# Optimization experiments

Measured on AMD Instinct MI355X. Metric: run time of the kernel, lower is better.

Reference implementation:

```python
import jax, jax.numpy as jnp
import numpy as np

B, A, NBH, F, G, H = 8, 512, 64, 128, 50, 8
DH = F // H
CUTOFF = 5.0


def setup_inputs() -> dict:
    key = jax.random.key(0)
    ks = jax.random.split(key, 13)
    x = jax.random.normal(ks[0], (B, A, F), jnp.float32)
    e = jax.random.normal(ks[1], (B, A, F), jnp.float32)
    t = jax.random.normal(ks[2], (B, F), jnp.float32)
    # distances in [0, 1.2*cutoff] so some pairs fall outside the cutoff
    r_ij = jax.random.uniform(ks[3], (B, A, NBH), jnp.float32) * (1.2 * CUTOFF)
    f_ij = jax.random.normal(ks[4], (B, A, NBH, G), jnp.float32)
    neighbors = jax.random.randint(ks[5], (B, A, NBH), 0, A, jnp.int32)
    neighbor_mask = jax.random.randint(ks[6], (B, A, NBH), 0, 2, jnp.int32).astype(bool)
    sF = 1.0 / np.sqrt(F).astype(np.float32)
    W_filt = jax.random.normal(ks[7], (G, F), jnp.float32) * (1.0 / np.sqrt(G).astype(np.float32))
    b_filt = jnp.zeros((F,), jnp.float32)
    Wq = jax.random.normal(ks[8], (F, F), jnp.float32) * sF
    Wk = jax.random.normal(ks[9], (F, F), jnp.float32) * sF
    Wv = jax.random.normal(ks[10], (F, F), jnp.float32) * sF
    Wo = jax.random.normal(ks[11], (F, F), jnp.float32) * sF
    bo = jnp.zeros((F,), jnp.float32)
    return dict(e=e, x=x, t=t, r_ij=r_ij, f_ij=f_ij,
                W_filt=W_filt, b_filt=b_filt, Wq=Wq, Wk=Wk, Wv=Wv, Wo=Wo, bo=bo,
                neighbors=neighbors, neighbor_mask=neighbor_mask)


def reference(e, x, t, r_ij, f_ij, W_filt, b_filt, Wq, Wk, Wv, Wo, bo,
              neighbors, neighbor_mask):
    # ---- filter network + cosine cutoff: W (B, A, NBH, F) ----
    W = f_ij @ W_filt + b_filt
    C = 0.5 * (jnp.cos(jnp.pi * r_ij / CUTOFF) + 1.0)
    C = C * (r_ij < CUTOFF).astype(x.dtype)           # (B, A, NBH)
    W = W * C[..., None]

    # ---- neighbor gather: nbh (B, A, NBH, F) ----
    bidx = jnp.arange(B)[:, None, None]
    nbh = x[bidx, neighbors]                           # irregular gather
    nbh = nbh * W                                      # filter-modulated messages

    # ---- EgoAttention: central atom queries its neighbors ----
    q = (x @ Wq).reshape(B, A, H, DH)                  # bahd
    k = (nbh @ Wk).reshape(B, A, NBH, H, DH)           # banhd
    v = (nbh @ Wv).reshape(B, A, NBH, H, DH)
    scale = np.float32(1.0 / np.sqrt(DH))
    scores = jnp.einsum('bahd,banhd->bahn', q, k) * scale
    scores = jnp.where(neighbor_mask[:, :, None, :], scores, jnp.float32(-1e9))
    attn = jax.nn.softmax(scores, axis=-1)             # over neighbors
    msg = jnp.einsum('bahn,banhd->bahd', attn, v).reshape(B, A, F)
    v_out = msg @ Wo + bo

    # ---- residual (apply_transition_function=False branch) ----
    return x + v_out
```

## Files before the change

kernel.cpp:

```cpp
#include <hip/hip_runtime.h>
#include <math.h>

#define BB 8
#define AA 512
#define NBH 64
#define FF 128
#define GG 50
#define CUTOFF 5.0f

typedef __attribute__((ext_vector_type(8)))  short bf16x8;
typedef __attribute__((ext_vector_type(4)))  float f32x4;
typedef __attribute__((ext_vector_type(16))) float f32x16;

#define MST 136

#define WKV_ELEMS (4*8*64*8)
#define WQO_ELEMS (8*4*64*8)
#define WF_ELEMS  (4*4*64*8)

__device__ __forceinline__ short f2bf(float f) {
    union { float f; unsigned u; } v; v.f = f;
    unsigned r = v.u + 0x7fffu + ((v.u >> 16) & 1u);
    return (short)(r >> 16);
}
__device__ __forceinline__ short f2bf_fast(float f) {
    return (short)((__float_as_uint(f) + 0x8000u) >> 16);
}
__device__ __forceinline__ unsigned int pk2bf(float a, float b) {
    unsigned int ua = __float_as_uint(a) + 0x8000u;
    unsigned int ub = __float_as_uint(b) + 0x8000u;
    return __builtin_amdgcn_perm(ub, ua, 0x07060302u);
}
__device__ __forceinline__ bf16x8 ld_f8_bfpk(const float* p) {
    const float2* p2 = (const float2*)p;
    float2 a = p2[0], b = p2[1], c = p2[2], d = p2[3];
    union { unsigned int u[4]; bf16x8 v; } r;
    r.u[0] = pk2bf(a.x, a.y);
    r.u[1] = pk2bf(b.x, b.y);
    r.u[2] = pk2bf(c.x, c.y);
    r.u[3] = pk2bf(d.x, d.y);
    return r.v;
}
__device__ __forceinline__ int swz(int n) { return ((n >> 3) & 3) << 3; }

__device__ __forceinline__ float row16_sum(float x) {
    int t;
    t = __builtin_amdgcn_update_dpp(0, __float_as_int(x), 0x128, 0xf, 0xf, true); x += __int_as_float(t);
    t = __builtin_amdgcn_update_dpp(0, __float_as_int(x), 0x124, 0xf, 0xf, true); x += __int_as_float(t);
    t = __builtin_amdgcn_update_dpp(0, __float_as_int(x), 0x122, 0xf, 0xf, true); x += __int_as_float(t);
    t = __builtin_amdgcn_update_dpp(0, __float_as_int(x), 0x121, 0xf, 0xf, true); x += __int_as_float(t);
    return x;
}

__global__ void prep_kernel(const float* __restrict__ Wk,
                            const float* __restrict__ Wv,
                            const float* __restrict__ Wq,
                            const float* __restrict__ Wo,
                            const float* __restrict__ Wf,
                            const float* __restrict__ b_filt,
                            short* __restrict__ ws)
{
    int gid = blockIdx.x * blockDim.x + threadIdx.x;
    if (gid < 2 * WKV_ELEMS) {
        const float* src = (gid < WKV_ELEMS) ? Wk : Wv;
        int idx = gid & (WKV_ELEMS - 1);
        int j = idx & 7, l = (idx >> 3) & 63, rest = idx >> 9;
        int s = rest & 7, w = rest >> 3;
        int k = 16 * s + ((l >> 5) << 3) + j;
        int n = 32 * w + (l & 31);
        ws[gid] = f2bf(src[k * FF + n]);
    } else if (gid < 2 * WKV_ELEMS + 2 * WQO_ELEMS) {
        int idx2 = gid - 2 * WKV_ELEMS;
        const float* src = (idx2 < WQO_ELEMS) ? Wq : Wo;
        int idx = idx2 & (WQO_ELEMS - 1);
        int j = idx & 7, l = (idx >> 3) & 63, rest = idx >> 9;
        int s = rest & 3, c = rest >> 2;
        int k = 32 * s + (l >> 4) * 8 + j;
        int n = 16 * c + (l & 15);
        ws[gid] = f2bf(src[k * FF + n]);
    } else {
        int idx = gid - 2 * WKV_ELEMS - 2 * WQO_ELEMS;
        int j = idx & 7, l = (idx >> 3) & 63, rest = idx >> 9;
        int s = rest & 3, w = rest >> 2;
        int k = 16 * s + ((l >> 5) << 3) + j;
        int n = 32 * w + (l & 31);
        float v = (k < GG) ? Wf[k * FF + n] : (k == GG ? b_filt[n] : 0.0f);
        ws[gid] = f2bf(v);
    }
}

__global__ __launch_bounds__(256, 4)
void tdt_main(const float* __restrict__ x,
              const float* __restrict__ r_ij,
              const float* __restrict__ f_ij,
              const float* __restrict__ bo,
              const int*   __restrict__ neighbors,
              const int*   __restrict__ nmask,
              const short* __restrict__ WkB,
              const short* __restrict__ WvB,
              const short* __restrict__ WqB,
              const short* __restrict__ WoB,
              const short* __restrict__ WfB,
              float* __restrict__ out)
{
    const int ba   = blockIdx.x;
    const int b    = ba >> 9;
    const int tid  = threadIdx.x;
    const int lane = tid & 63;
    const int w    = tid >> 6;
    const int l15  = lane & 15;
    const int quad = lane >> 4;
    const int l31  = lane & 31;
    const int khalf = (lane >> 5) << 3;
    const int w5_4  = (lane >> 5) * 4;

    __shared__ short M_s[NBH * MST];
    __shared__ short msg_bf[FF];

    const float* xrow = x + (size_t)ba * FF;
    const float* xb   = x + (size_t)b * AA * FF;
    const size_t bao  = (size_t)ba;

    int   nbr_reg = neighbors[bao * NBH + lane];
    float C_reg;
    {
        float r = r_ij[bao * NBH + lane];
        float c = 0.5f * (__cosf((float)M_PI * r * (1.0f / CUTOFF)) + 1.0f);
        C_reg = (r < CUTOFF) ? c : 0.0f;
    }
    unsigned long long mask64 = __ballot(nmask[bao * NBH + lane] != 0);

    float qvm;
    {
        bf16x8 xa[4];
#pragma unroll
        for (int s = 0; s < 4; ++s)
            xa[s] = ld_f8_bfpk(xrow + 32 * s + quad * 8);
        float qv0, qv1;
#pragma unroll
        for (int ct = 0; ct < 2; ++ct) {
            int cg = 2 * w + ct;
            f32x4 z = {0.f, 0.f, 0.f, 0.f};
#pragma unroll
            for (int s = 0; s < 4; ++s) {
                bf16x8 bq = *(const bf16x8*)&WqB[((cg * 4 + s) * 64 + lane) * 8];
                z = __builtin_amdgcn_mfma_f32_16x16x32_bf16(xa[s], bq, z, 0, 0, 0);
            }
            if (ct == 0) qv0 = z[0]; else qv1 = z[0];
        }
        qvm = ((lane >> 4) & 1) ? qv1 : qv0;
    }

    {
        f32x16 wacc[2];
#pragma unroll
        for (int mt = 0; mt < 2; ++mt)
#pragma unroll
            for (int r = 0; r < 16; ++r) wacc[mt][r] = 0.0f;

        const float* fm0 = f_ij + bao * (size_t)(NBH * GG) + (size_t)l31 * GG;
#pragma unroll
        for (int s = 0; s < 4; ++s) {
            bf16x8 bfw = *(const bf16x8*)&WfB[((w * 4 + s) * 64 + lane) * 8];
#pragma unroll
            for (int mt = 0; mt < 2; ++mt) {
                const float* fm = fm0 + mt * 32 * GG;
                bf16x8 fa;
                if (s < 3) {
                    fa = ld_f8_bfpk(fm + 16 * s + khalf);
                } else {
#pragma unroll
                    for (int jj = 0; jj < 8; ++jj) fa[jj] = 0;
                    if (lane < 32) {
                        fa[0] = f2bf_fast(fm[48]);
                        fa[1] = f2bf_fast(fm[49]);
                        fa[2] = (short)0x3F80;
                    }
                }
                wacc[mt] = __builtin_amdgcn_mfma_f32_32x32x16_bf16(fa, bfw, wacc[mt], 0, 0, 0);
            }
        }

        int c = 32 * w + l31;
#pragma unroll
        for (int mt = 0; mt < 2; ++mt) {
#pragma unroll
            for (int r = 0; r < 16; ++r) {
                int   n   = 32 * mt + (r & 3) + 8 * (r >> 2) + w5_4;
                int   nbn = __shfl(nbr_reg, n, 64);
                float cn  = __shfl(C_reg, n, 64);
                float xv  = xb[(size_t)nbn * FF + c];
                M_s[n * MST + (c ^ swz(n))] = f2bf_fast(wacc[mt][r] * cn * xv);
            }
        }
    }
    __syncthreads();

    float sc[2][16];
    float inv;
    {
#pragma unroll
        for (int mt = 0; mt < 2; ++mt) {
            f32x16 kacc;
#pragma unroll
            for (int r = 0; r < 16; ++r) kacc[r] = 0.0f;
            int m = 32 * mt + l31;
#pragma unroll
            for (int s = 0; s < 8; ++s) {
                bf16x8 bk = *(const bf16x8*)&WkB[((w * 8 + s) * 64 + lane) * 8];
                int kb = 16 * s + khalf;
                bf16x8 ma = *(const bf16x8*)&M_s[m * MST + (kb ^ swz(m))];
                kacc = __builtin_amdgcn_mfma_f32_32x32x16_bf16(ma, bk, kacc, 0, 0, 0);
            }
#pragma unroll
            for (int r = 0; r < 16; ++r) {
                float s = row16_sum(kacc[r] * qvm) * 0.25f;
                int n = 32 * mt + (r & 3) + 8 * (r >> 2) + w5_4;
                sc[mt][r] = ((mask64 >> n) & 1ull) ? s : -1e9f;
            }
        }
        float mx = -1e30f;
#pragma unroll
        for (int mt = 0; mt < 2; ++mt)
#pragma unroll
            for (int r = 0; r < 16; ++r) mx = fmaxf(mx, sc[mt][r]);
        mx = fmaxf(mx, __shfl_xor(mx, 32, 64));
        float sum = 0.0f;
#pragma unroll
        for (int mt = 0; mt < 2; ++mt)
#pragma unroll
            for (int r = 0; r < 16; ++r) {
                float e = __expf(sc[mt][r] - mx);
                sc[mt][r] = e;
                sum += e;
            }
        sum += __shfl_xor(sum, 32, 64);
        inv = 1.0f / sum;
    }

    {
        float acc = 0.0f;
#pragma unroll
        for (int mt = 0; mt < 2; ++mt) {
            f32x16 vacc;
#pragma unroll
            for (int r = 0; r < 16; ++r) vacc[r] = 0.0f;
            int m = 32 * mt + l31;
#pragma unroll
            for (int s = 0; s < 8; ++s) {
                bf16x8 bv = *(const bf16x8*)&WvB[((w * 8 + s) * 64 + lane) * 8];
                int kb = 16 * s + khalf;
                bf16x8 ma = *(const bf16x8*)&M_s[m * MST + (kb ^ swz(m))];
                vacc = __builtin_amdgcn_mfma_f32_32x32x16_bf16(ma, bv, vacc, 0, 0, 0);
            }
#pragma unroll
            for (int r = 0; r < 16; ++r)
                acc = fmaf(sc[mt][r], vacc[r], acc);
        }
        acc += __shfl_xor(acc, 32, 64);
        if (lane < 32) msg_bf[32 * w + l31] = f2bf_fast(acc * inv);
    }
    __syncthreads();

    {
        bf16x8 mga[4];
#pragma unroll
        for (int s = 0; s < 4; ++s)
            mga[s] = *(const bf16x8*)&msg_bf[s * 32 + quad * 8];
#pragma unroll
        for (int ct = 0; ct < 2; ++ct) {
            int cg = 2 * w + ct;
            f32x4 z = {0.f, 0.f, 0.f, 0.f};
#pragma unroll
            for (int s = 0; s < 4; ++s) {
                bf16x8 bw = *(const bf16x8*)&WoB[((cg * 4 + s) * 64 + lane) * 8];
                z = __builtin_amdgcn_mfma_f32_16x16x32_bf16(mga[s], bw, z, 0, 0, 0);
            }
            if (quad == 0) {
                int col = cg * 16 + l15;
                out[bao * FF + col] = z[0] + xrow[col] + bo[col];
            }
        }
    }
}

extern "C" void kernel_launch(void* const* d_in, const int* in_sizes, int n_in,
                              void* d_out, int out_size, void* d_ws, size_t ws_size,
                              hipStream_t stream) {
    const float* x      = (const float*)d_in[1];
    const float* r_ij   = (const float*)d_in[3];
    const float* f_ij   = (const float*)d_in[4];
    const float* W_filt = (const float*)d_in[5];
    const float* b_filt = (const float*)d_in[6];
    const float* Wq     = (const float*)d_in[7];
    const float* Wk     = (const float*)d_in[8];
    const float* Wv     = (const float*)d_in[9];
    const float* Wo     = (const float*)d_in[10];
    const float* bo     = (const float*)d_in[11];
    const int*   nbr    = (const int*)d_in[12];
    const int*   msk    = (const int*)d_in[13];
    float* out = (float*)d_out;

    short* ws  = (short*)d_ws;
    short* WkB = ws;
    short* WvB = ws + WKV_ELEMS;
    short* WqB = ws + 2 * WKV_ELEMS;
    short* WoB = ws + 2 * WKV_ELEMS + WQO_ELEMS;
    short* WfB = ws + 2 * WKV_ELEMS + 2 * WQO_ELEMS;

    int prep_total = 2 * WKV_ELEMS + 2 * WQO_ELEMS + WF_ELEMS;
    hipLaunchKernelGGL(prep_kernel, dim3(prep_total / 256), dim3(256), 0, stream,
                       Wk, Wv, Wq, Wo, W_filt, b_filt, ws);
    hipLaunchKernelGGL(tdt_main, dim3(BB * AA), dim3(256), 0, stream,
                       x, r_ij, f_ij, bo, nbr, msk,
                       WkB, WvB, WqB, WoB, WfB, out);
}
```

Measured before the change: 164.2 us.

## Pre-convert x to bf16, fuse K/V MFMA passes, drop softmax max subtraction

The prep kernel now also converts x to a bf16 copy in the workspace, so the neighbor gather reads 2-byte values instead of 4-byte floats. The separate K-score/softmax and V-accumulate phases are merged into one loop that loads the M_s fragments once and feeds both MFMA chains. The softmax max subtraction is removed and exp is applied directly to the scores, with masked entries set to zero. This cuts LDS reads and gather bandwidth, but it adds an extra pass over x in the prep kernel and risks exp overflow if scores grow large.

Result: no change. 163.1 us (-0.7%).

```diff
diff --git a/kernel.cpp b/kernel.cpp
--- a/kernel.cpp
+++ b/kernel.cpp
@@ -17,6 +17,7 @@
 #define WKV_ELEMS (4*8*64*8)
 #define WQO_ELEMS (8*4*64*8)
 #define WF_ELEMS  (4*4*64*8)
+#define XB_ELEMS  (BB*AA*FF)
 
 __device__ __forceinline__ short f2bf(float f) {
     union { float f; unsigned u; } v; v.f = f;
@@ -58,6 +59,7 @@
                             const float* __restrict__ Wo,
                             const float* __restrict__ Wf,
                             const float* __restrict__ b_filt,
+                            const float* __restrict__ x,
                             short* __restrict__ ws)
 {
     int gid = blockIdx.x * blockDim.x + threadIdx.x;
@@ -78,7 +80,7 @@
         int k = 32 * s + (l >> 4) * 8 + j;
         int n = 16 * c + (l & 15);
         ws[gid] = f2bf(src[k * FF + n]);
-    } else {
+    } else if (gid < 2 * WKV_ELEMS + 2 * WQO_ELEMS + WF_ELEMS) {
         int idx = gid - 2 * WKV_ELEMS - 2 * WQO_ELEMS;
         int j = idx & 7, l = (idx >> 3) & 63, rest = idx >> 9;
         int s = rest & 3, w = rest >> 2;
@@ -86,6 +88,9 @@
         int n = 32 * w + (l & 31);
         float v = (k < GG) ? Wf[k * FF + n] : (k == GG ? b_filt[n] : 0.0f);
         ws[gid] = f2bf(v);
+    } else {
+        int idx = gid - 2 * WKV_ELEMS - 2 * WQO_ELEMS - WF_ELEMS;
+        ws[gid] = f2bf(x[idx]);
     }
 }
 
@@ -101,6 +106,7 @@
               const short* __restrict__ WqB,
               const short* __restrict__ WoB,
               const short* __restrict__ WfB,
+              const short* __restrict__ xB,
               float* __restrict__ out)
 {
     const int ba   = blockIdx.x;
@@ -118,8 +124,8 @@
     __shared__ short msg_bf[FF];
 
     const float* xrow = x + (size_t)ba * FF;
-    const float* xb   = x + (size_t)b * AA * FF;
-    const size_t bao  = (size_t)ba;
+    const unsigned short* xbu = (const unsigned short*)xB + (size_t)b * AA * FF;
+    const size_t bao = (size_t)ba;
 
     int   nbr_reg = neighbors[bao * NBH + lane];
     float C_reg;
@@ -132,10 +138,11 @@
 
     float qvm;
     {
+        const short* xbrow = &xB[(size_t)ba * FF];
         bf16x8 xa[4];
 #pragma unroll
         for (int s = 0; s < 4; ++s)
-            xa[s] = ld_f8_bfpk(xrow + 32 * s + quad * 8);
+            xa[s] = *(const bf16x8*)&xbrow[32 * s + quad * 8];
         float qv0, qv1;
 #pragma unroll
         for (int ct = 0; ct < 2; ++ct) {
@@ -148,23 +155,21 @@
             }
             if (ct == 0) qv0 = z[0]; else qv1 = z[0];
         }
-        qvm = ((lane >> 4) & 1) ? qv1 : qv0;
-    }
-
-    {
-        f32x16 wacc[2];
-#pragma unroll
-        for (int mt = 0; mt < 2; ++mt)
-#pragma unroll
-            for (int r = 0; r < 16; ++r) wacc[mt][r] = 0.0f;
-
+        qvm = (((lane >> 4) & 1) ? qv1 : qv0) * 0.25f;
+    }
+
+    {
         const float* fm0 = f_ij + bao * (size_t)(NBH * GG) + (size_t)l31 * GG;
-#pragma unroll
-        for (int s = 0; s < 4; ++s) {
-            bf16x8 bfw = *(const bf16x8*)&WfB[((w * 4 + s) * 64 + lane) * 8];
-#pragma unroll
-            for (int mt = 0; mt < 2; ++mt) {
-                const float* fm = fm0 + mt * 32 * GG;
+        int c = 32 * w + l31;
+#pragma unroll
+        for (int mt = 0; mt < 2; ++mt) {
+            f32x16 wacc;
+#pragma unroll
+            for (int r = 0; r < 16; ++r) wacc[r] = 0.0f;
+            const float* fm = fm0 + mt * 32 * GG;
+#pragma unroll
+            for (int s = 0; s < 4; ++s) {
+                bf16x8 bfw = *(const bf16x8*)&WfB[((w * 4 + s) * 64 + lane) * 8];
                 bf16x8 fa;
                 if (s < 3) {
                     fa = ld_f8_bfpk(fm + 16 * s + khalf);
@@ -177,89 +182,56 @@
                         fa[2] = (short)0x3F80;
                     }
                 }
-                wacc[mt] = __builtin_amdgcn_mfma_f32_32x32x16_bf16(fa, bfw, wacc[mt], 0, 0, 0);
-            }
-        }
-
-        int c = 32 * w + l31;
-#pragma unroll
-        for (int mt = 0; mt < 2; ++mt) {
+                wacc = __builtin_amdgcn_mfma_f32_32x32x16_bf16(fa, bfw, wacc, 0, 0, 0);
+            }
 #pragma unroll
             for (int r = 0; r < 16; ++r) {
                 int   n   = 32 * mt + (r & 3) + 8 * (r >> 2) + w5_4;
                 int   nbn = __shfl(nbr_reg, n, 64);
                 float cn  = __shfl(C_reg, n, 64);
-                float xv  = xb[(size_t)nbn * FF + c];
-                M_s[n * MST + (c ^ swz(n))] = f2bf_fast(wacc[mt][r] * cn * xv);
+                float xv  = __uint_as_float((unsigned)xbu[(size_t)nbn * FF + c] << 16);
+                M_s[n * MST + (c ^ swz(n))] = f2bf_fast(wacc[r] * cn * xv);
             }
         }
     }
     __syncthreads();
 
-    float sc[2][16];
-    float inv;
-    {
-#pragma unroll
-        for (int mt = 0; mt < 2; ++mt) {
-            f32x16 kacc;
-#pragma unroll
-            for (int r = 0; r < 16; ++r) kacc[r] = 0.0f;
-            int m = 32 * mt + l31;
-#pragma unroll
-            for (int s = 0; s < 8; ++s) {
-                bf16x8 bk = *(const bf16x8*)&WkB[((w * 8 + s) * 64 + lane) * 8];
-                int kb = 16 * s + khalf;
-                bf16x8 ma = *(const bf16x8*)&M_s[m * MST + (kb ^ swz(m))];
-                kacc = __builtin_amdgcn_mfma_f32_32x32x16_bf16(ma, bk, kacc, 0, 0, 0);
-            }
-#pragma unroll
-            for (int r = 0; r < 16; ++r) {
-                float s = row16_sum(kacc[r] * qvm) * 0.25f;
-                int n = 32 * mt + (r & 3) + 8 * (r >> 2) + w5_4;
-                sc[mt][r] = ((mask64 >> n) & 1ull) ? s : -1e9f;
-            }
-        }
-        float mx = -1e30f;
-#pragma unroll
-        for (int mt = 0; mt < 2; ++mt)
-#pragma unroll
-            for (int r = 0; r < 16; ++r) mx = fmaxf(mx, sc[mt][r]);
-        mx = fmaxf(mx, __shfl_xor(mx, 32, 64));
-        float sum = 0.0f;
-#pragma unroll
-        for (int mt = 0; mt < 2; ++mt)
-#pragma unroll
-            for (int r = 0; r < 16; ++r) {
-                float e = __expf(sc[mt][r] - mx);
-                sc[mt][r] = e;
-                sum += e;
-            }
-        sum += __shfl_xor(sum, 32, 64);
-        inv = 1.0f / sum;
-    }
-
-    {
-        float acc = 0.0f;
-#pragma unroll
-        for (int mt = 0; mt < 2; ++mt) {
-            f32x16 vacc;
-#pragma unroll
-            for (int r = 0; r < 16; ++r) vacc[r] = 0.0f;
-            int m = 32 * mt + l31;
-#pragma unroll
-            for (int s = 0; s < 8; ++s) {
-                bf16x8 bv = *(const bf16x8*)&WvB[((w * 8 + s) * 64 + lane) * 8];
-                int kb = 16 * s + khalf;
-                bf16x8 ma = *(const bf16x8*)&M_s[m * MST + (kb ^ swz(m))];
-                vacc = __builtin_amdgcn_mfma_f32_32x32x16_bf16(ma, bv, vacc, 0, 0, 0);
-            }
-#pragma unroll
-            for (int r = 0; r < 16; ++r)
-                acc = fmaf(sc[mt][r], vacc[r], acc);
-        }
-        acc += __shfl_xor(acc, 32, 64);
-        if (lane < 32) msg_bf[32 * w + l31] = f2bf_fast(acc * inv);
-    }
+    float sum = 0.0f, acc = 0.0f;
+#pragma unroll
+    for (int mt = 0; mt < 2; ++mt) {
+        int m = 32 * mt + l31;
+        bf16x8 ma[8];
+#pragma unroll
+        for (int s = 0; s < 8; ++s)
+            ma[s] = *(const bf16x8*)&M_s[m * MST + ((16 * s + khalf) ^ swz(m))];
+        f32x16 kacc;
+#pragma unroll
+        for (int r = 0; r < 16; ++r) kacc[r] = 0.0f;
+#pragma unroll
+        for (int s = 0; s < 8; ++s) {
+            bf16x8 bk = *(const bf16x8*)&WkB[((w * 8 + s) * 64 + lane) * 8];
+            kacc = __builtin_amdgcn_mfma_f32_32x32x16_bf16(ma[s], bk, kacc, 0, 0, 0);
+        }
+        f32x16 vacc;
+#pragma unroll
+        for (int r = 0; r < 16; ++r) vacc[r] = 0.0f;
+#pragma unroll
+        for (int s = 0; s < 8; ++s) {
+            bf16x8 bv = *(const bf16x8*)&WvB[((w * 8 + s) * 64 + lane) * 8];
+            vacc = __builtin_amdgcn_mfma_f32_32x32x16_bf16(ma[s], bv, vacc, 0, 0, 0);
+        }
+#pragma unroll
+        for (int r = 0; r < 16; ++r) {
+            float sr = row16_sum(kacc[r] * qvm);
+            int   n  = 32 * mt + (r & 3) + 8 * (r >> 2) + w5_4;
+            float e  = ((mask64 >> n) & 1ull) ? __expf(sr) : 0.0f;
+            sum += e;
+            acc  = fmaf(e, vacc[r], acc);
+        }
+    }
+    sum += __shfl_xor(sum, 32, 64);
+    acc += __shfl_xor(acc, 32, 64);
+    if (lane < 32) msg_bf[32 * w + l31] = f2bf_fast(acc / sum);
     __syncthreads();
 
     {
@@ -307,11 +279,12 @@
     short* WqB = ws + 2 * WKV_ELEMS;
     short* WoB = ws + 2 * WKV_ELEMS + WQO_ELEMS;
     short* WfB = ws + 2 * WKV_ELEMS + 2 * WQO_ELEMS;
-
-    int prep_total = 2 * WKV_ELEMS + 2 * WQO_ELEMS + WF_ELEMS;
+    short* xB  = ws + 2 * WKV_ELEMS + 2 * WQO_ELEMS + WF_ELEMS;
+
+    int prep_total = 2 * WKV_ELEMS + 2 * WQO_ELEMS + WF_ELEMS + XB_ELEMS;
     hipLaunchKernelGGL(prep_kernel, dim3(prep_total / 256), dim3(256), 0, stream,
-                       Wk, Wv, Wq, Wo, W_filt, b_filt, ws);
+                       Wk, Wv, Wq, Wo, W_filt, b_filt, x, ws);
     hipLaunchKernelGGL(tdt_main, dim3(BB * AA), dim3(256), 0, stream,
                        x, r_ij, f_ij, bo, nbr, msk,
-                       WkB, WvB, WqB, WoB, WfB, out);
-}
+                       WkB, WvB, WqB, WoB, WfB, xB, out);
+}
```
